# Kernel tuning notes

Hardware: AMD Instinct MI355X
Metric: run time of the kernel (lower is better)

## Reference

```python
import jax, jax.numpy as jnp
import numpy as np

B, OBS, H, M, L1, T, A = 16384, 376, 512, 8, 3, 50, 17  # L1 = num_layers - 1
LOG_SQRT_2PI = 0.5 * np.log(2.0 * np.pi).astype(np.float32)


def setup_inputs() -> dict:
    key = jax.random.key(0)
    ks = jax.random.split(key, 16)
    s = lambda fan: 1.0 / np.sqrt(fan).astype(np.float32)
    return {
        "x": jax.random.normal(ks[0], (B, OBS), jnp.float32),
        "task_idx": jax.random.randint(ks[1], (B,), 0, T, jnp.int64),
        "enc_W1": jax.random.normal(ks[2], (OBS, H), jnp.float32) * s(OBS),
        "enc_b1": jnp.zeros((H,), jnp.float32),
        "enc_W2": jax.random.normal(ks[3], (H, H), jnp.float32) * s(H),
        "enc_b2": jnp.zeros((H,), jnp.float32),
        "task_emb": jax.random.normal(ks[4], (T, H), jnp.float32),
        "a_rW": jax.random.normal(ks[5], (L1, H, M * M), jnp.float32) * s(H),
        "a_rb": jnp.zeros((L1, M * M), jnp.float32),
        "c_rW": jax.random.normal(ks[6], (L1, H, M * M), jnp.float32) * s(H),
        "c_rb": jnp.zeros((L1, M * M), jnp.float32),
        "a_W": jax.random.normal(ks[7], (L1, M, H, H), jnp.float32) * s(H),
        "a_b": jnp.zeros((L1, M, H), jnp.float32),
        "a_Wf": jax.random.normal(ks[8], (M, H, A), jnp.float32) * 0.01,
        "a_bf": jnp.zeros((M, A), jnp.float32),
        "c_W": jax.random.normal(ks[9], (L1, M, H, H), jnp.float32) * s(H),
        "c_b": jnp.zeros((L1, M, H), jnp.float32),
        "c_Wf": jax.random.normal(ks[10], (M, H, 1), jnp.float32) * s(H),
        "c_bf": jnp.zeros((M, 1), jnp.float32),
        "actor_logstd": jnp.zeros((1, A), jnp.float32),
    }


def _routing(context, rW, rb):
    # context: [B,H]; rW: [L1,H,M*M] -> list of [B,M,M] softmax routing probs
    rel = jax.nn.relu(context)
    probs = []
    for l in range(L1):
        logits = (rel @ rW[l] + rb[l]).reshape(-1, M, M)
        probs.append(jax.nn.softmax(logits, axis=2))
    return probs


def _base(f_s, probs, W, b, Wf, bf):
    # f_s: [B,H]; W: [L1,M,H,H]; Wf: [M,H,out]
    g = jnp.broadcast_to(f_s[:, None, :], (f_s.shape[0], M, H))  # [B,M,H]
    for l in range(L1):
        outs = jax.nn.relu(jnp.einsum("bmh,mhk->bmk", g, W[l]) + b[l])  # [B,M,H]
        g = jnp.einsum("bij,bjh->bih", probs[l], outs)  # soft combine
    final = jnp.einsum("bmh,mhk->bmk", g, Wf) + bf  # [B,M,out]
    return final.sum(axis=1)


def reference(x, task_idx, enc_W1, enc_b1, enc_W2, enc_b2, task_emb,
              a_rW, a_rb, c_rW, c_rb, a_W, a_b, a_Wf, a_bf,
              c_W, c_b, c_Wf, c_bf, actor_logstd):
    f_s = jnp.tanh(jnp.tanh(x @ enc_W1 + enc_b1) @ enc_W2 + enc_b2)  # [B,H]
    h_z = task_emb[task_idx]  # [B,H]
    context = f_s * h_z

    value = _base(f_s, _routing(context, c_rW, c_rb), c_W, c_b, c_Wf, c_bf)  # [B,1]
    mean = _base(f_s, _routing(context, a_rW, a_rb), a_W, a_b, a_Wf, a_bf)   # [B,A]

    # deterministic action (sample=False): action = mean
    logstd = jnp.broadcast_to(actor_logstd, mean.shape)
    log_prob = (-logstd - LOG_SQRT_2PI).sum(axis=1)          # N.log_prob(mean).sum(1)
    entropy = (0.5 + LOG_SQRT_2PI + logstd).sum(axis=1)
    # concat (action, log_prob, entropy, value) -> [B, A+3]
    return jnp.concatenate([mean, log_prob[:, None], entropy[:, None], value], axis=1)
```

## Files before the change

### kernel.cpp

```cpp
#include <hip/hip_runtime.h>
#include <hip/hip_bf16.h>

typedef float f32x4 __attribute__((ext_vector_type(4)));
typedef float f32x2 __attribute__((ext_vector_type(2)));
typedef int   i32x4 __attribute__((ext_vector_type(4)));
typedef int   i32x8 __attribute__((ext_vector_type(8)));

#define LOG_SQRT_2PI 0.91893853320467274f

static constexpr int BSZ  = 16384;
static constexpr int OBSN = 376;
static constexpr int HD   = 512;
static constexpr int NACT = 17;

__device__ __forceinline__ unsigned char f2fp8(float v) {
  return (unsigned char)(__builtin_amdgcn_cvt_pk_fp8_f32(v, v, 0, false) & 0xFF);
}

__device__ __forceinline__ void xcd_map(int id, int gx, int gy, int& bx, int& by, int& bz) {
  int p = id & 7, l = id >> 3;
  bx = l % gx;
  int g = (l / gx) * 8 + p;
  by = g % gy;
  bz = g / gy;
}


__global__ void k_cvt_pad8(const float* __restrict__ src, unsigned char* __restrict__ dst) {
  long i = (long)blockIdx.x * 256 + threadIdx.x;
  if (i >= (long)BSZ * HD) return;
  long r = i >> 9;
  int  c = (int)(i & 511);
  dst[i] = f2fp8(c < OBSN ? src[r * OBSN + c] : 0.f);
}

__global__ void k_packT8(const float* __restrict__ src, unsigned char* __restrict__ dst,
                         int K, int N, int Kpad, long sstride, long dstride, float scale) {
  __shared__ float t[32][33];
  src += (long)blockIdx.z * sstride;
  dst += (long)blockIdx.z * dstride;
  int k0 = blockIdx.y * 32, n0 = blockIdx.x * 32;
#pragma unroll
  for (int ii = 0; ii < 4; ++ii) {
    int i = ii * 8 + threadIdx.y;
    int k = k0 + i, n = n0 + threadIdx.x;
    t[i][threadIdx.x] = (k < K && n < N) ? src[(long)k * N + n] : 0.f;
  }
  __syncthreads();
#pragma unroll
  for (int ii = 0; ii < 4; ++ii) {
    int i = ii * 8 + threadIdx.y;
    int n = n0 + i, k = k0 + threadIdx.x;
    if (n < N && k < Kpad) dst[(long)n * Kpad + k] = f2fp8(scale * t[threadIdx.x][i]);
  }
}

__global__ void k_packw8(const float* __restrict__ aW, const float* __restrict__ cW,
                         unsigned char* __restrict__ dst) {
  __shared__ float t[32][33];
  const int z = blockIdx.z;
  const int layer = z >> 4, zz = z & 15, net = zz >> 3, m = zz & 7;
  const float* src = (net ? aW : cW) + (long)(layer * 8 + m) * 262144;
  unsigned char* d = dst + (long)z * 262144;
  int k0 = blockIdx.y * 32, n0 = blockIdx.x * 32;
#pragma unroll
  for (int ii = 0; ii < 4; ++ii) {
    int i = ii * 8 + threadIdx.y;
    t[i][threadIdx.x] = src[(long)(k0 + i) * 512 + n0 + threadIdx.x];
  }
  __syncthreads();
#pragma unroll
  for (int ii = 0; ii < 4; ++ii) {
    int i = ii * 8 + threadIdx.y;
    d[(long)(n0 + i) * 512 + k0 + threadIdx.x] = f2fp8(16.f * t[threadIdx.x][i]);
  }
}

__global__ void k_pack_lb(const float* __restrict__ a_b, const float* __restrict__ c_b,
                          float* __restrict__ lb) {
  int i = blockIdx.x * 256 + threadIdx.x;
  if (i >= 24576) return;
  int layer = i >> 13, zz = (i >> 9) & 15, n = i & 511;
  int net = zz >> 3, m = zz & 7;
  lb[i] = (net ? a_b : c_b)[(layer * 8 + m) * 512 + n];
}

__global__ void k_packwf8(const float* __restrict__ aWf, const float* __restrict__ cWf,
                          unsigned char* __restrict__ dsta, unsigned char* __restrict__ dstc) {
  int i = blockIdx.x * 256 + threadIdx.x;
  int n = i >> 12, k = i & 4095;
  dsta[i] = (n < NACT) ? f2fp8(64.f * aWf[(long)k * NACT + n]) : (unsigned char)0;
  dstc[i] = (n < 1)    ? f2fp8(64.f * cWf[k])                  : (unsigned char)0;
}

__global__ void k_pack_rb(const float* __restrict__ a_rb, const float* __restrict__ c_rb,
                          float* __restrict__ rb) {
  int i = threadIdx.x;
  rb[i] = (i < 192) ? a_rb[i] : c_rb[i - 192];
}

__global__ void k_sum_bf(const float* __restrict__ a_bf, const float* __restrict__ c_bf,
                         float* __restrict__ sa, float* __restrict__ sc) {
  int a = threadIdx.x;
  if (a < NACT) { float s = 0.f; for (int m = 0; m < 8; ++m) s += a_bf[m * NACT + a]; sa[a] = s; }
  if (a == 0)   { float s = 0.f; for (int m = 0; m < 8; ++m) s += c_bf[m];            sc[0] = s; }
}

template <int OP>
__global__ __launch_bounds__(256, 4)
void k_gemm8(const unsigned char* __restrict__ A, const unsigned char* __restrict__ Bt,
             void* __restrict__ Cv, const float* __restrict__ bias,
             int N, int K, int lda, int ldc, int gx, int gy,
             int a_zoff, int b_zoff, int c_zoff, int bias_zoff,
             const int* __restrict__ tidx, const float* __restrict__ temb,
             unsigned char* __restrict__ out2) {
  __shared__ alignas(16) unsigned char sA[128 * 128];
  __shared__ alignas(16) unsigned char sB[128 * 128];
  int bx, by, z;
  xcd_map(blockIdx.x, gx, gy, bx, by, z);
  A  += (long)z * a_zoff;
  Bt += (long)z * b_zoff;
  const int tid  = threadIdx.x;
  const int wave = tid >> 6, lane = tid & 63;
  const int wr = (wave >> 1) * 64, wc = (wave & 1) * 64;
  const int row0 = by * 128, col0 = bx * 128;
  const int lcol = lane & 15, quad = lane >> 4;
  const int sw7 = lcol & 7;
  const int c0 = ((2 * quad)     ^ sw7) * 16;
  const int c1 = ((2 * quad + 1) ^ sw7) * 16;
  const int raA0 = (wr + lcol) * 128 + c0, raA1 = (wr + lcol) * 128 + c1;
  const int rbB0 = (wc + lcol) * 128 + c0, rbB1 = (wc + lcol) * 128 + c1;
  int aOff[4], bOff[4];
#pragma unroll
  for (int i = 0; i < 4; ++i) {
    int u = i * 256 + tid;
    int r = u >> 3, gc = (u & 7) ^ (r & 7);
    aOff[i] = (row0 + r) * lda + gc * 16;
    bOff[i] = (col0 + r) * K + gc * 16;
  }

  f32x4 acc[4][4] = {};

  for (int kt = 0; kt < K; kt += 128) {
#pragma unroll
    for (int i = 0; i < 4; ++i)
      __builtin_amdgcn_global_load_lds(
          (const __attribute__((address_space(1))) void*)(A + aOff[i] + kt),
          (__attribute__((address_space(3))) void*)&sA[i * 4096 + tid * 16], 16, 0, 0);
#pragma unroll
    for (int i = 0; i < 4; ++i)
      __builtin_amdgcn_global_load_lds(
          (const __attribute__((address_space(1))) void*)(Bt + bOff[i] + kt),
          (__attribute__((address_space(3))) void*)&sB[i * 4096 + tid * 16], 16, 0, 0);
    __syncthreads();
    i32x8 bv[4];
#pragma unroll
    for (int ni = 0; ni < 4; ++ni) {
      i32x4 blo = *(const i32x4*)&sB[rbB0 + ni * 2048];
      i32x4 bhi = *(const i32x4*)&sB[rbB1 + ni * 2048];
      bv[ni] = (i32x8){blo[0], blo[1], blo[2], blo[3], bhi[0], bhi[1], bhi[2], bhi[3]};
    }
#pragma unroll
    for (int mi = 0; mi < 4; ++mi) {
      i32x4 alo = *(const i32x4*)&sA[raA0 + mi * 2048];
      i32x4 ahi = *(const i32x4*)&sA[raA1 + mi * 2048];
      i32x8 af = (i32x8){alo[0], alo[1], alo[2], alo[3], ahi[0], ahi[1], ahi[2], ahi[3]};
#pragma unroll
      for (int ni = 0; ni < 4; ++ni)
        acc[mi][ni] = __builtin_amdgcn_mfma_scale_f32_16x16x128_f8f6f4(
            bv[ni], af, acc[mi][ni], 0, 0, 0, 0x7F, 0, 0x7F);
    }
    __syncthreads();
  }

  if (OP == 0) {
#pragma unroll
    for (int ni = 0; ni < 4; ++ni) {
      int colb = col0 + wc + ni * 16 + quad * 4;
      float4 bw = *(const float4*)&bias[(long)z * bias_zoff + colb];
      int chunk = (wc >> 4) + ni;
#pragma unroll
      for (int mi = 0; mi < 4; ++mi) {
        int rowl = wr + mi * 16 + lcol;
        float v0 = fmaxf(acc[mi][ni][0] * 0.0625f + bw.x, 0.f);
        float v1 = fmaxf(acc[mi][ni][1] * 0.0625f + bw.y, 0.f);
        float v2 = fmaxf(acc[mi][ni][2] * 0.0625f + bw.z, 0.f);
        float v3 = fmaxf(acc[mi][ni][3] * 0.0625f + bw.w, 0.f);
        unsigned d = __builtin_amdgcn_cvt_pk_fp8_f32(v0, v1, 0, false);
        d = __builtin_amdgcn_cvt_pk_fp8_f32(v2, v3, d, true);
        *(unsigned*)&sA[rowl * 128 + ((chunk ^ (rowl & 7)) << 4) + quad * 4] = d;
      }
    }
    __syncthreads();
#pragma unroll
    for (int i2 = 0; i2 < 4; ++i2) {
      int u = i2 * 256 + tid;
      int r = u >> 3, p = u & 7;
      i32x4 v = *(const i32x4*)&sA[r * 128 + p * 16];
      int chl = p ^ (r & 7);
      long idx = (long)(row0 + r) * ldc + (long)z * c_zoff + col0 + chl * 16;
      *(i32x4*)&((unsigned char*)Cv)[idx] = v;
    }
    return;
  }

#pragma unroll
  for (int ni = 0; ni < 4; ++ni) {
    int colb = col0 + wc + ni * 16 + quad * 4;
    if (colb >= N) continue;
    float4 bw = *(const float4*)&bias[(long)z * bias_zoff + colb];
#pragma unroll
    for (int mi = 0; mi < 4; ++mi) {
      int rowg = row0 + wr + mi * 16 + lcol;
      float v0 = acc[mi][ni][0] * 0.0625f + bw.x;
      float v1 = acc[mi][ni][1] * 0.0625f + bw.y;
      float v2 = acc[mi][ni][2] * 0.0625f + bw.z;
      float v3 = acc[mi][ni][3] * 0.0625f + bw.w;
      long idx = (long)rowg * ldc + (long)z * c_zoff + colb;
      if (OP == 1) {
        float t0 = tanhf(v0), t1 = tanhf(v1), t2 = tanhf(v2), t3 = tanhf(v3);
        unsigned d = __builtin_amdgcn_cvt_pk_fp8_f32(t0, t1, 0, false);
        d = __builtin_amdgcn_cvt_pk_fp8_f32(t2, t3, d, true);
        *(unsigned*)&((unsigned char*)Cv)[idx] = d;
      } else if (OP == 5) {
        float t0 = tanhf(v0), t1 = tanhf(v1), t2 = tanhf(v2), t3 = tanhf(v3);
        unsigned d = __builtin_amdgcn_cvt_pk_fp8_f32(t0, t1, 0, false);
        d = __builtin_amdgcn_cvt_pk_fp8_f32(t2, t3, d, true);
        *(unsigned*)&((unsigned char*)Cv)[idx] = d;
        int tk = tidx[rowg];
        float4 te = *(const float4*)&temb[(long)tk * HD + colb];
        unsigned e = __builtin_amdgcn_cvt_pk_fp8_f32(fmaxf(t0 * te.x, 0.f), fmaxf(t1 * te.y, 0.f), 0, false);
        e = __builtin_amdgcn_cvt_pk_fp8_f32(fmaxf(t2 * te.z, 0.f), fmaxf(t3 * te.w, 0.f), e, true);
        *(unsigned*)&out2[idx] = e;
      } else if (OP == 4) {
        float mx = fmaxf(fmaxf(v0, v1), fmaxf(v2, v3));
        mx = fmaxf(mx, __shfl_xor(mx, 16));
        float e0 = __expf(v0 - mx), e1 = __expf(v1 - mx), e2 = __expf(v2 - mx), e3 = __expf(v3 - mx);
        float s = e0 + e1 + e2 + e3;
        s += __shfl_xor(s, 16);
        float inv = 1.f / s;
        *(float4*)&((float*)Cv)[idx] = make_float4(e0 * inv, e1 * inv, e2 * inv, e3 * inv);
      }
    }
  }
}

__global__ __launch_bounds__(256)
void k_combine8(const unsigned char* __restrict__ outs, const float* __restrict__ probs,
                unsigned char* __restrict__ g, int poffC, int poffA) {
  __shared__ float P[4][64];
  const int w = threadIdx.x >> 6, l = threadIdx.x & 63;
  const int net = blockIdx.x & 1;
  const long b = (long)(blockIdx.x >> 1) * 4 + w;
  P[w][l] = probs[b * 384 + (net ? poffA : poffC) + l];
  __syncthreads();
  const unsigned char* ob = outs + b * 8192 + net * 4096 + l * 8;
  float o[8][8];
#pragma unroll
  for (int j = 0; j < 8; ++j) {
    uint2 v = *(const uint2*)(ob + j * 512);
    f32x2 p01 = __builtin_amdgcn_cvt_pk_f32_fp8(v.x, false);
    f32x2 p23 = __builtin_amdgcn_cvt_pk_f32_fp8(v.x, true);
    f32x2 p45 = __builtin_amdgcn_cvt_pk_f32_fp8(v.y, false);
    f32x2 p67 = __builtin_amdgcn_cvt_pk_f32_fp8(v.y, true);
    o[j][0] = p01.x; o[j][1] = p01.y; o[j][2] = p23.x; o[j][3] = p23.y;
    o[j][4] = p45.x; o[j][5] = p45.y; o[j][6] = p67.x; o[j][7] = p67.y;
  }
  unsigned char* gb = g + b * 8192 + net * 4096 + l * 8;
#pragma unroll
  for (int i = 0; i < 8; ++i) {
    float a[8] = {};
#pragma unroll
    for (int j = 0; j < 8; ++j) {
      float pw = P[w][i * 8 + j];
#pragma unroll
      for (int c = 0; c < 8; ++c) a[c] += pw * o[j][c];
    }
    unsigned int lo = __builtin_amdgcn_cvt_pk_fp8_f32(a[0], a[1], 0, false);
    lo = __builtin_amdgcn_cvt_pk_fp8_f32(a[2], a[3], lo, true);
    unsigned int hi = __builtin_amdgcn_cvt_pk_fp8_f32(a[4], a[5], 0, false);
    hi = __builtin_amdgcn_cvt_pk_fp8_f32(a[6], a[7], hi, true);
    *(uint2*)(gb + i * 512) = make_uint2(lo, hi);
  }
}

template <int NOUT>
__global__ __launch_bounds__(256)
void k_head8(const unsigned char* __restrict__ A, const unsigned char* __restrict__ Bt,
             const float* __restrict__ bsum, float* __restrict__ out, int lda, int ooff) {
  __shared__ alignas(16) unsigned char sA[64 * 64];
  __shared__ alignas(16) unsigned char sB[32 * 64];
  const int tid = threadIdx.x;
  const int wave = tid >> 6, lane = tid & 63;
  const int row0 = blockIdx.x * 64;
  const int lcol = lane & 15, quad = lane >> 4;
  const int sw = (lcol >> 1) & 3;
  const int co0 = (((quad >> 1)    ) ^ sw) * 16 + (quad & 1) * 8;
  const int co1 = (((quad >> 1) + 2) ^ sw) * 16 + (quad & 1) * 8;
  f32x4 acc[2] = {};

  for (int kt = 0; kt < 4096; kt += 64) {
    {
      int r = tid >> 2, gc = (tid & 3) ^ ((tid >> 3) & 3);
      const unsigned char* ga = A + (long)(row0 + r) * lda + kt + gc * 16;
      __builtin_amdgcn_global_load_lds((const __attribute__((address_space(1))) void*)ga,
                                       (__attribute__((address_space(3))) void*)&sA[tid * 16], 16, 0, 0);
    }
    if (tid < 128) {
      int r = tid >> 2, gc = (tid & 3) ^ ((tid >> 3) & 3);
      const unsigned char* gb = Bt + (long)r * 4096 + kt + gc * 16;
      __builtin_amdgcn_global_load_lds((const __attribute__((address_space(1))) void*)gb,
                                       (__attribute__((address_space(3))) void*)&sB[tid * 16], 16, 0, 0);
    }
    __syncthreads();
    long af[2], bv[2][2];
    int ra = (wave * 16 + lcol) * 64;
    af[0] = *(const long*)&sA[ra + co0];
    af[1] = *(const long*)&sA[ra + co1];
#pragma unroll
    for (int ni = 0; ni < 2; ++ni) {
      int rb = (ni * 16 + lcol) * 64;
      bv[0][ni] = *(const long*)&sB[rb + co0];
      bv[1][ni] = *(const long*)&sB[rb + co1];
    }
#pragma unroll
    for (int kk = 0; kk < 2; ++kk)
#pragma unroll
      for (int ni = 0; ni < 2; ++ni)
        acc[ni] = __builtin_amdgcn_mfma_f32_16x16x32_fp8_fp8(af[kk], bv[kk][ni], acc[ni], 0, 0, 0);
    __syncthreads();
  }

#pragma unroll
  for (int ni = 0; ni < 2; ++ni) {
    int col = ni * 16 + lcol;
    if (col >= NOUT) continue;
#pragma unroll
    for (int r = 0; r < 4; ++r) {
      int row = row0 + wave * 16 + quad * 4 + r;
      out[(long)row * 20 + ooff + col] = acc[ni][r] * 0.015625f + bsum[col];
    }
  }
}

__global__ void k_logstd(const float* __restrict__ ls, float* __restrict__ out) {
  float lp = 0.f, ent = 0.f;
#pragma unroll
  for (int a = 0; a < NACT; ++a) {
    float v = ls[a];
    lp  += -v - LOG_SQRT_2PI;
    ent += 0.5f + LOG_SQRT_2PI + v;
  }
  long b = (long)blockIdx.x * 256 + threadIdx.x;
  if (b < BSZ) { out[b * 20 + 17] = lp; out[b * 20 + 18] = ent; }
}


extern "C" void kernel_launch(void* const* d_in, const int* in_sizes, int n_in,
                              void* d_out, int out_size, void* d_ws, size_t ws_size,
                              hipStream_t stream) {
  const float* x        = (const float*)d_in[0];
  const int*   task_idx = (const int*)d_in[1];
  const float* enc_W1   = (const float*)d_in[2];
  const float* enc_b1   = (const float*)d_in[3];
  const float* enc_W2   = (const float*)d_in[4];
  const float* enc_b2   = (const float*)d_in[5];
  const float* task_emb = (const float*)d_in[6];
  const float* a_rW     = (const float*)d_in[7];
  const float* a_rb     = (const float*)d_in[8];
  const float* c_rW     = (const float*)d_in[9];
  const float* c_rb     = (const float*)d_in[10];
  const float* a_W      = (const float*)d_in[11];
  const float* a_b      = (const float*)d_in[12];
  const float* a_Wf     = (const float*)d_in[13];
  const float* a_bf     = (const float*)d_in[14];
  const float* c_W      = (const float*)d_in[15];
  const float* c_b      = (const float*)d_in[16];
  const float* c_Wf     = (const float*)d_in[17];
  const float* c_bf     = (const float*)d_in[18];
  const float* logstd   = (const float*)d_in[19];
  float* out = (float*)d_out;

  char* ws = (char*)d_ws;
  size_t off = 0;
  auto carve = [&](size_t bytes) {
    char* p = ws + off;
    off += (bytes + 255) & ~(size_t)255;
    return p;
  };
  unsigned char* W8 = (unsigned char*)carve((size_t)48 * 262144);
  unsigned char* W1T8 = (unsigned char*)carve((size_t)512 * 512);
  unsigned char* W2T8 = (unsigned char*)carve((size_t)512 * 512);
  unsigned char* rWT8 = (unsigned char*)carve((size_t)384 * 512);
  float* rball = (float*)carve(384 * 4);
  float* lb    = (float*)carve(3 * 16 * 512 * 4);
  unsigned char* WfaT8 = (unsigned char*)carve((size_t)32 * 4096);
  unsigned char* WfcT8 = (unsigned char*)carve((size_t)32 * 4096);
  float* bfa   = (float*)carve(128 * 4);
  float* bfc   = (float*)carve(128 * 4);
  unsigned char* fs8 = (unsigned char*)carve((size_t)BSZ * HD);
  float* lgt   = (float*)carve((size_t)BSZ * 384 * 4);

  size_t remain = (ws_size > off) ? (ws_size - off) : 0;
  int Bc = 2048;
  for (int cand = BSZ; cand > 2048; cand >>= 1)
    if ((size_t)2 * cand * 8192 <= remain) { Bc = cand; break; }
  size_t half = (size_t)Bc * 8192;
  unsigned char* bufA8 = (unsigned char*)carve(half);
  unsigned char* bufB8 = (unsigned char*)carve(half);
  unsigned char* x8   = bufA8;
  unsigned char* h18  = bufB8;
  unsigned char* rel8 = bufA8;

  dim3 tb(32, 8);

  k_cvt_pad8<<<(int)(((long)BSZ * HD + 255) / 256), 256, 0, stream>>>(x, x8);
  k_packT8<<<dim3(16, 16, 1), tb, 0, stream>>>(enc_W1, W1T8, OBSN, 512, 512, 0, 0, 16.f);
  k_packT8<<<dim3(16, 16, 1), tb, 0, stream>>>(enc_W2, W2T8, 512, 512, 512, 0, 0, 16.f);
  k_packT8<<<dim3(2, 16, 3),  tb, 0, stream>>>(a_rW, rWT8,             512, 64, 512, 512 * 64, 64 * 512, 16.f);
  k_packT8<<<dim3(2, 16, 3),  tb, 0, stream>>>(c_rW, rWT8 + 192 * 512, 512, 64, 512, 512 * 64, 64 * 512, 16.f);
  k_packw8<<<dim3(16, 16, 48), tb, 0, stream>>>(a_W, c_W, W8);
  k_pack_lb<<<96, 256, 0, stream>>>(a_b, c_b, lb);
  k_packwf8<<<512, 256, 0, stream>>>(a_Wf, c_Wf, WfaT8, WfcT8);
  k_pack_rb<<<1, 384, 0, stream>>>(a_rb, c_rb, rball);
  k_sum_bf<<<1, 32, 0, stream>>>(a_bf, c_bf, bfa, bfc);

  const int GY = BSZ / 128;
  k_gemm8<1><<<4 * GY, 256, 0, stream>>>(x8, W1T8, h18, enc_b1, 512, 512, 512, 512,
                                         4, GY, 0, 0, 0, 0, nullptr, nullptr, nullptr);
  k_gemm8<5><<<4 * GY, 256, 0, stream>>>(h18, W2T8, fs8, enc_b2, 512, 512, 512, 512,
                                         4, GY, 0, 0, 0, 0, task_idx, task_emb, rel8);
  k_gemm8<4><<<3 * GY, 256, 0, stream>>>(rel8, rWT8, lgt, rball, 384, 512, 512, 384,
                                         3, GY, 0, 0, 0, 0, nullptr, nullptr, nullptr);

  const size_t wlz = (size_t)16 * 262144;
  for (int c0 = 0; c0 < BSZ; c0 += Bc) {
    const unsigned char* fs_c = fs8 + (long)c0 * 512;
    const float* pr_c  = lgt + (long)c0 * 384;
    float*       out_c = out + (long)c0 * 20;
    const int gy = Bc / 128;

    k_gemm8<0><<<64 * gy, 256, 0, stream>>>(fs_c, W8, bufA8, lb, 8192, 512, 512, 8192,
                                            64, gy, 0, 0, 0, 0, nullptr, nullptr, nullptr);
    k_combine8<<<Bc / 2, 256, 0, stream>>>(bufA8, pr_c, bufB8, 192 + 0, 0);
    k_gemm8<0><<<64 * gy, 256, 0, stream>>>(bufB8, W8 + wlz, bufA8, lb + 8192,
                                            512, 512, 8192, 8192, 4, gy, 512, 262144, 512, 512,
                                            nullptr, nullptr, nullptr);
    k_combine8<<<Bc / 2, 256, 0, stream>>>(bufA8, pr_c, bufB8, 192 + 64, 64);
    k_gemm8<0><<<64 * gy, 256, 0, stream>>>(bufB8, W8 + 2 * wlz, bufA8, lb + 16384,
                                            512, 512, 8192, 8192, 4, gy, 512, 262144, 512, 512,
                                            nullptr, nullptr, nullptr);
    k_combine8<<<Bc / 2, 256, 0, stream>>>(bufA8, pr_c, bufB8, 192 + 128, 128);
    k_head8<1><<<Bc / 64, 256, 0, stream>>>(bufB8, WfcT8, bfc, out_c, 8192, 19);
    k_head8<NACT><<<Bc / 64, 256, 0, stream>>>(bufB8 + 4096, WfaT8, bfa, out_c, 8192, 0);
  }

  k_logstd<<<BSZ / 256, 256, 0, stream>>>(logstd, out);
}
```

Before: 768.3 us.

## Fuse per-expert GEMM with routing combine in a single expert-layer kernel

Replaces the per-layer pair of an expert GEMM (k_gemm8<0>) and a separate combine kernel with one kernel, k_gemmF. Each block holds a 64-row slab, with one wave per module, and keeps all 8 modules' ReLU outputs for a 128-column slice in LDS. It then applies the soft routing combine there before writing g. This removes the round trip of the [B,8,H] intermediate through global memory and three kernel launches per chunk. In exchange it uses 128KB of shared memory per block and reads weights directly from global memory without LDS staging, which may limit occupancy and raise weight-load traffic.

```diff
diff --git a/kernel.cpp b/kernel.cpp
--- a/kernel.cpp
+++ b/kernel.cpp
@@ -15,6 +15,11 @@
 
 __device__ __forceinline__ unsigned char f2fp8(float v) {
   return (unsigned char)(__builtin_amdgcn_cvt_pk_fp8_f32(v, v, 0, false) & 0xFF);
+}
+
+__device__ __forceinline__ void gl16(const unsigned char* g, unsigned char* l) {
+  __builtin_amdgcn_global_load_lds((const __attribute__((address_space(1))) void*)g,
+                                   (__attribute__((address_space(3))) void*)l, 16, 0, 0);
 }
 
 __device__ __forceinline__ void xcd_map(int id, int gx, int gy, int& bx, int& by, int& bz) {
@@ -111,15 +116,12 @@
 void k_gemm8(const unsigned char* __restrict__ A, const unsigned char* __restrict__ Bt,
              void* __restrict__ Cv, const float* __restrict__ bias,
              int N, int K, int lda, int ldc, int gx, int gy,
-             int a_zoff, int b_zoff, int c_zoff, int bias_zoff,
              const int* __restrict__ tidx, const float* __restrict__ temb,
              unsigned char* __restrict__ out2) {
   __shared__ alignas(16) unsigned char sA[128 * 128];
   __shared__ alignas(16) unsigned char sB[128 * 128];
   int bx, by, z;
   xcd_map(blockIdx.x, gx, gy, bx, by, z);
-  A  += (long)z * a_zoff;
-  Bt += (long)z * b_zoff;
   const int tid  = threadIdx.x;
   const int wave = tid >> 6, lane = tid & 63;
   const int wr = (wave >> 1) * 64, wc = (wave & 1) * 64;
@@ -143,15 +145,9 @@
 
   for (int kt = 0; kt < K; kt += 128) {
 #pragma unroll
-    for (int i = 0; i < 4; ++i)
-      __builtin_amdgcn_global_load_lds(
-          (const __attribute__((address_space(1))) void*)(A + aOff[i] + kt),
-          (__attribute__((address_space(3))) void*)&sA[i * 4096 + tid * 16], 16, 0, 0);
-#pragma unroll
-    for (int i = 0; i < 4; ++i)
-      __builtin_amdgcn_global_load_lds(
-          (const __attribute__((address_space(1))) void*)(Bt + bOff[i] + kt),
-          (__attribute__((address_space(3))) void*)&sB[i * 4096 + tid * 16], 16, 0, 0);
+    for (int i = 0; i < 4; ++i) gl16(A + aOff[i] + kt, &sA[i * 4096 + tid * 16]);
+#pragma unroll
+    for (int i = 0; i < 4; ++i) gl16(Bt + bOff[i] + kt, &sB[i * 4096 + tid * 16]);
     __syncthreads();
     i32x8 bv[4];
 #pragma unroll
@@ -173,42 +169,11 @@
     __syncthreads();
   }
 
-  if (OP == 0) {
-#pragma unroll
-    for (int ni = 0; ni < 4; ++ni) {
-      int colb = col0 + wc + ni * 16 + quad * 4;
-      float4 bw = *(const float4*)&bias[(long)z * bias_zoff + colb];
-      int chunk = (wc >> 4) + ni;
-#pragma unroll
-      for (int mi = 0; mi < 4; ++mi) {
-        int rowl = wr + mi * 16 + lcol;
-        float v0 = fmaxf(acc[mi][ni][0] * 0.0625f + bw.x, 0.f);
-        float v1 = fmaxf(acc[mi][ni][1] * 0.0625f + bw.y, 0.f);
-        float v2 = fmaxf(acc[mi][ni][2] * 0.0625f + bw.z, 0.f);
-        float v3 = fmaxf(acc[mi][ni][3] * 0.0625f + bw.w, 0.f);
-        unsigned d = __builtin_amdgcn_cvt_pk_fp8_f32(v0, v1, 0, false);
-        d = __builtin_amdgcn_cvt_pk_fp8_f32(v2, v3, d, true);
-        *(unsigned*)&sA[rowl * 128 + ((chunk ^ (rowl & 7)) << 4) + quad * 4] = d;
-      }
-    }
-    __syncthreads();
-#pragma unroll
-    for (int i2 = 0; i2 < 4; ++i2) {
-      int u = i2 * 256 + tid;
-      int r = u >> 3, p = u & 7;
-      i32x4 v = *(const i32x4*)&sA[r * 128 + p * 16];
-      int chl = p ^ (r & 7);
-      long idx = (long)(row0 + r) * ldc + (long)z * c_zoff + col0 + chl * 16;
-      *(i32x4*)&((unsigned char*)Cv)[idx] = v;
-    }
-    return;
-  }
-
 #pragma unroll
   for (int ni = 0; ni < 4; ++ni) {
     int colb = col0 + wc + ni * 16 + quad * 4;
     if (colb >= N) continue;
-    float4 bw = *(const float4*)&bias[(long)z * bias_zoff + colb];
+    float4 bw = *(const float4*)&bias[colb];
 #pragma unroll
     for (int mi = 0; mi < 4; ++mi) {
       int rowg = row0 + wr + mi * 16 + lcol;
@@ -216,7 +181,7 @@
       float v1 = acc[mi][ni][1] * 0.0625f + bw.y;
       float v2 = acc[mi][ni][2] * 0.0625f + bw.z;
       float v3 = acc[mi][ni][3] * 0.0625f + bw.w;
-      long idx = (long)rowg * ldc + (long)z * c_zoff + colb;
+      long idx = (long)rowg * ldc + colb;
       if (OP == 1) {
         float t0 = tanhf(v0), t1 = tanhf(v1), t2 = tanhf(v2), t3 = tanhf(v3);
         unsigned d = __builtin_amdgcn_cvt_pk_fp8_f32(t0, t1, 0, false);
@@ -245,42 +210,144 @@
   }
 }
 
-__global__ __launch_bounds__(256)
-void k_combine8(const unsigned char* __restrict__ outs, const float* __restrict__ probs,
-                unsigned char* __restrict__ g, int poffC, int poffA) {
-  __shared__ float P[4][64];
-  const int w = threadIdx.x >> 6, l = threadIdx.x & 63;
-  const int net = blockIdx.x & 1;
-  const long b = (long)(blockIdx.x >> 1) * 4 + w;
-  P[w][l] = probs[b * 384 + (net ? poffA : poffC) + l];
+template <int AMODE>
+__global__ __launch_bounds__(512, 2)
+void k_gemmF(const unsigned char* __restrict__ A, const unsigned char* __restrict__ W,
+             const float* __restrict__ lb, const float* __restrict__ probs,
+             unsigned char* __restrict__ g, int gy, int poffC, int poffA) {
+  __shared__ alignas(16) unsigned char sA[65536];
+  __shared__ alignas(16) unsigned char sO[65536];
+  int hb, slab, net;
+  xcd_map(blockIdx.x, 4, gy, hb, slab, net);
+  const int tid = threadIdx.x;
+  const int w = tid >> 6, lane = tid & 63;
+  const int lcol = lane & 15, quad = lane >> 4;
+  const int row0 = slab * 64;
+  const int h0 = hb * 128;
+  const int sw7 = lcol & 7;
+  const int c0 = ((2 * quad)     ^ sw7) * 16;
+  const int c1 = ((2 * quad + 1) ^ sw7) * 16;
+  const unsigned char* Wz = W + (long)(net * 8 + w) * 262144 + (h0 + lcol) * 512 + quad * 32;
+
+  f32x4 acc[4][8] = {};
+
+  if (AMODE == 0) {
+#pragma unroll
+    for (int i = 0; i < 4; ++i) {
+      int u = i * 512 + tid;
+      int r = (u >> 3) & 63, ch = (u & 7) ^ (r & 7);
+      gl16(A + (row0 + r) * 512 + (u >> 9) * 128 + ch * 16, &sA[u * 16]);
+    }
+    __syncthreads();
+#pragma unroll
+    for (int t = 0; t < 4; ++t) {
+      const int kt = t * 128;
+      const unsigned char* sAb = sA + t * 8192;
+      i32x8 bv[8];
+#pragma unroll
+      for (int ni = 0; ni < 8; ++ni) {
+        i32x4 lo = *(const i32x4*)(Wz + ni * 8192 + kt);
+        i32x4 hi = *(const i32x4*)(Wz + ni * 8192 + kt + 16);
+        bv[ni] = (i32x8){lo[0], lo[1], lo[2], lo[3], hi[0], hi[1], hi[2], hi[3]};
+      }
+#pragma unroll
+      for (int mi = 0; mi < 4; ++mi) {
+        int ra = (mi * 16 + lcol) * 128;
+        i32x4 lo = *(const i32x4*)&sAb[ra + c0];
+        i32x4 hi = *(const i32x4*)&sAb[ra + c1];
+        i32x8 af = (i32x8){lo[0], lo[1], lo[2], lo[3], hi[0], hi[1], hi[2], hi[3]};
+#pragma unroll
+        for (int ni = 0; ni < 8; ++ni)
+          acc[mi][ni] = __builtin_amdgcn_mfma_scale_f32_16x16x128_f8f6f4(
+              bv[ni], af, acc[mi][ni], 0, 0, 0, 0x7F, 0, 0x7F);
+      }
+    }
+    __syncthreads();
+  } else {
+#pragma unroll 1
+    for (int t = 0; t < 4; ++t) {
+      const int kt = t * 128;
+#pragma unroll
+      for (int i = 0; i < 8; ++i) {
+        int u = i * 512 + tid;
+        int j = u >> 9, rem = u & 511;
+        int r = rem >> 3, ch = (rem & 7) ^ (r & 7);
+        gl16(A + (long)(row0 + r) * 8192 + net * 4096 + j * 512 + kt + ch * 16, &sA[u * 16]);
+      }
+      __syncthreads();
+      const unsigned char* sAb = sA + (w << 13);
+      i32x8 bv[8];
+#pragma unroll
+      for (int ni = 0; ni < 8; ++ni) {
+        i32x4 lo = *(const i32x4*)(Wz + ni * 8192 + kt);
+        i32x4 hi = *(const i32x4*)(Wz + ni * 8192 + kt + 16);
+        bv[ni] = (i32x8){lo[0], lo[1], lo[2], lo[3], hi[0], hi[1], hi[2], hi[3]};
+      }
+#pragma unroll
+      for (int mi = 0; mi < 4; ++mi) {
+        int ra = (mi * 16 + lcol) * 128;
+        i32x4 lo = *(const i32x4*)&sAb[ra + c0];
+        i32x4 hi = *(const i32x4*)&sAb[ra + c1];
+        i32x8 af = (i32x8){lo[0], lo[1], lo[2], lo[3], hi[0], hi[1], hi[2], hi[3]};
+#pragma unroll
+        for (int ni = 0; ni < 8; ++ni)
+          acc[mi][ni] = __builtin_amdgcn_mfma_scale_f32_16x16x128_f8f6f4(
+              bv[ni], af, acc[mi][ni], 0, 0, 0, 0x7F, 0, 0x7F);
+      }
+      __syncthreads();
+    }
+  }
+
+#pragma unroll
+  for (int ni = 0; ni < 8; ++ni) {
+    int col = ni * 16 + quad * 4;
+    float4 bw = *(const float4*)&lb[(net * 8 + w) * 512 + h0 + col];
+#pragma unroll
+    for (int mi = 0; mi < 4; ++mi) {
+      int row = mi * 16 + lcol;
+      float v0 = fmaxf(acc[mi][ni][0] * 0.0625f + bw.x, 0.f);
+      float v1 = fmaxf(acc[mi][ni][1] * 0.0625f + bw.y, 0.f);
+      float v2 = fmaxf(acc[mi][ni][2] * 0.0625f + bw.z, 0.f);
+      float v3 = fmaxf(acc[mi][ni][3] * 0.0625f + bw.w, 0.f);
+      unsigned d = __builtin_amdgcn_cvt_pk_fp8_f32(v0, v1, 0, false);
+      d = __builtin_amdgcn_cvt_pk_fp8_f32(v2, v3, d, true);
+      *(unsigned*)&sO[(w << 13) + row * 128 + ((ni ^ (row & 7)) << 4) + quad * 4] = d;
+    }
+  }
   __syncthreads();
-  const unsigned char* ob = outs + b * 8192 + net * 4096 + l * 8;
-  float o[8][8];
-#pragma unroll
-  for (int j = 0; j < 8; ++j) {
-    uint2 v = *(const uint2*)(ob + j * 512);
-    f32x2 p01 = __builtin_amdgcn_cvt_pk_f32_fp8(v.x, false);
-    f32x2 p23 = __builtin_amdgcn_cvt_pk_f32_fp8(v.x, true);
-    f32x2 p45 = __builtin_amdgcn_cvt_pk_f32_fp8(v.y, false);
-    f32x2 p67 = __builtin_amdgcn_cvt_pk_f32_fp8(v.y, true);
-    o[j][0] = p01.x; o[j][1] = p01.y; o[j][2] = p23.x; o[j][3] = p23.y;
-    o[j][4] = p45.x; o[j][5] = p45.y; o[j][6] = p67.x; o[j][7] = p67.y;
-  }
-  unsigned char* gb = g + b * 8192 + net * 4096 + l * 8;
-#pragma unroll
-  for (int i = 0; i < 8; ++i) {
-    float a[8] = {};
+
+  const int rb = lane >> 3, hp = lane & 7;
+  const int poff = net ? poffA : poffC;
+#pragma unroll
+  for (int k = 0; k < 8; ++k) {
+    const int r = rb + k * 8;
+    const float* pr = &probs[(long)(row0 + r) * 384 + poff + w * 8];
+    float4 pA = *(const float4*)pr;
+    float4 pB = *(const float4*)(pr + 4);
+    float p8[8] = {pA.x, pA.y, pA.z, pA.w, pB.x, pB.y, pB.z, pB.w};
+    float ga[16] = {};
 #pragma unroll
     for (int j = 0; j < 8; ++j) {
-      float pw = P[w][i * 8 + j];
-#pragma unroll
-      for (int c = 0; c < 8; ++c) a[c] += pw * o[j][c];
-    }
-    unsigned int lo = __builtin_amdgcn_cvt_pk_fp8_f32(a[0], a[1], 0, false);
-    lo = __builtin_amdgcn_cvt_pk_fp8_f32(a[2], a[3], lo, true);
-    unsigned int hi = __builtin_amdgcn_cvt_pk_fp8_f32(a[4], a[5], 0, false);
-    hi = __builtin_amdgcn_cvt_pk_fp8_f32(a[6], a[7], hi, true);
-    *(uint2*)(gb + i * 512) = make_uint2(lo, hi);
+      i32x4 o4 = *(const i32x4*)&sO[(j << 13) + r * 128 + ((hp ^ rb) << 4)];
+      float pw = p8[j];
+#pragma unroll
+      for (int dw = 0; dw < 4; ++dw) {
+        f32x2 lo = __builtin_amdgcn_cvt_pk_f32_fp8((unsigned)o4[dw], false);
+        f32x2 hi = __builtin_amdgcn_cvt_pk_f32_fp8((unsigned)o4[dw], true);
+        ga[dw * 4 + 0] += pw * lo.x;
+        ga[dw * 4 + 1] += pw * lo.y;
+        ga[dw * 4 + 2] += pw * hi.x;
+        ga[dw * 4 + 3] += pw * hi.y;
+      }
+    }
+    i32x4 gg;
+#pragma unroll
+    for (int dw = 0; dw < 4; ++dw) {
+      unsigned d = __builtin_amdgcn_cvt_pk_fp8_f32(ga[dw * 4 + 0], ga[dw * 4 + 1], 0, false);
+      d = __builtin_amdgcn_cvt_pk_fp8_f32(ga[dw * 4 + 2], ga[dw * 4 + 3], d, true);
+      gg[dw] = (int)d;
+    }
+    *(i32x4*)&g[(long)(row0 + r) * 8192 + net * 4096 + w * 512 + h0 + hp * 16] = gg;
   }
 }
 
@@ -302,15 +369,11 @@
   for (int kt = 0; kt < 4096; kt += 64) {
     {
       int r = tid >> 2, gc = (tid & 3) ^ ((tid >> 3) & 3);
-      const unsigned char* ga = A + (long)(row0 + r) * lda + kt + gc * 16;
-      __builtin_amdgcn_global_load_lds((const __attribute__((address_space(1))) void*)ga,
-                                       (__attribute__((address_space(3))) void*)&sA[tid * 16], 16, 0, 0);
+      gl16(A + (long)(row0 + r) * lda + kt + gc * 16, &sA[tid * 16]);
     }
     if (tid < 128) {
       int r = tid >> 2, gc = (tid & 3) ^ ((tid >> 3) & 3);
-      const unsigned char* gb = Bt + (long)r * 4096 + kt + gc * 16;
-      __builtin_amdgcn_global_load_lds((const __attribute__((address_space(1))) void*)gb,
-                                       (__attribute__((address_space(3))) void*)&sB[tid * 16], 16, 0, 0);
+      gl16(Bt + (long)r * 4096 + kt + gc * 16, &sB[tid * 16]);
     }
     __syncthreads();
     long af[2], bv[2][2];
@@ -319,9 +382,9 @@
     af[1] = *(const long*)&sA[ra + co1];
 #pragma unroll
     for (int ni = 0; ni < 2; ++ni) {
-      int rb = (ni * 16 + lcol) * 64;
-      bv[0][ni] = *(const long*)&sB[rb + co0];
-      bv[1][ni] = *(const long*)&sB[rb + co1];
+      int rbq = (ni * 16 + lcol) * 64;
+      bv[0][ni] = *(const long*)&sB[rbq + co0];
+      bv[1][ni] = *(const long*)&sB[rbq + co1];
     }
 #pragma unroll
     for (int kk = 0; kk < 2; ++kk)
@@ -427,32 +490,26 @@
 
   const int GY = BSZ / 128;
   k_gemm8<1><<<4 * GY, 256, 0, stream>>>(x8, W1T8, h18, enc_b1, 512, 512, 512, 512,
-                                         4, GY, 0, 0, 0, 0, nullptr, nullptr, nullptr);
+                                         4, GY, nullptr, nullptr, nullptr);
   k_gemm8<5><<<4 * GY, 256, 0, stream>>>(h18, W2T8, fs8, enc_b2, 512, 512, 512, 512,
-                                         4, GY, 0, 0, 0, 0, task_idx, task_emb, rel8);
+                                         4, GY, task_idx, task_emb, rel8);
   k_gemm8<4><<<3 * GY, 256, 0, stream>>>(rel8, rWT8, lgt, rball, 384, 512, 512, 384,
-                                         3, GY, 0, 0, 0, 0, nullptr, nullptr, nullptr);
+                                         3, GY, nullptr, nullptr, nullptr);
 
   const size_t wlz = (size_t)16 * 262144;
   for (int c0 = 0; c0 < BSZ; c0 += Bc) {
     const unsigned char* fs_c = fs8 + (long)c0 * 512;
     const float* pr_c  = lgt + (long)c0 * 384;
     float*       out_c = out + (long)c0 * 20;
-    const int gy = Bc / 128;
-
-    k_gemm8<0><<<64 * gy, 256, 0, stream>>>(fs_c, W8, bufA8, lb, 8192, 512, 512, 8192,
-                                            64, gy, 0, 0, 0, 0, nullptr, nullptr, nullptr);
-    k_combine8<<<Bc / 2, 256, 0, stream>>>(bufA8, pr_c, bufB8, 192 + 0, 0);
-    k_gemm8<0><<<64 * gy, 256, 0, stream>>>(bufB8, W8 + wlz, bufA8, lb + 8192,
-                                            512, 512, 8192, 8192, 4, gy, 512, 262144, 512, 512,
-                                            nullptr, nullptr, nullptr);
-    k_combine8<<<Bc / 2, 256, 0, stream>>>(bufA8, pr_c, bufB8, 192 + 64, 64);
-    k_gemm8<0><<<64 * gy, 256, 0, stream>>>(bufB8, W8 + 2 * wlz, bufA8, lb + 16384,
-                                            512, 512, 8192, 8192, 4, gy, 512, 262144, 512, 512,
-                                            nullptr, nullptr, nullptr);
-    k_combine8<<<Bc / 2, 256, 0, stream>>>(bufA8, pr_c, bufB8, 192 + 128, 128);
-    k_head8<1><<<Bc / 64, 256, 0, stream>>>(bufB8, WfcT8, bfc, out_c, 8192, 19);
-    k_head8<NACT><<<Bc / 64, 256, 0, stream>>>(bufB8 + 4096, WfaT8, bfa, out_c, 8192, 0);
+    const int gyF = Bc / 64;
+
+    k_gemmF<0><<<8 * gyF, 512, 0, stream>>>(fs_c, W8, lb, pr_c, bufA8, gyF, 192, 0);
+    k_gemmF<1><<<8 * gyF, 512, 0, stream>>>(bufA8, W8 + wlz, lb + 8192, pr_c, bufB8,
+                                            gyF, 192 + 64, 64);
+    k_gemmF<1><<<8 * gyF, 512, 0, stream>>>(bufB8, W8 + 2 * wlz, lb + 16384, pr_c, bufA8,
+                                            gyF, 192 + 128, 128);
+    k_head8<1><<<Bc / 64, 256, 0, stream>>>(bufA8, WfcT8, bfc, out_c, 8192, 19);
+    k_head8<NACT><<<Bc / 64, 256, 0, stream>>>(bufA8 + 4096, WfaT8, bfa, out_c, 8192, 0);
   }
 
   k_logstd<<<BSZ / 256, 256, 0, stream>>>(logstd, out);
```

Measured after the change: 1.154 ms. 50.2% more time.
